# Performance work log

Measured on AMD Instinct MI355X. Metric: run time of the kernel, lower is better.

## Reference

```python
import jax, jax.numpy as jnp
import numpy as np

PI = float(np.pi)


def _lsa_cols(cost):
    """Jonker-Volgenant / Hungarian on a square cost matrix (numpy float64).
    Returns col_ind such that (arange(n), col_ind) is the optimal assignment,
    matching scipy.optimize.linear_sum_assignment for a square matrix."""
    n = cost.shape[0]
    C = np.zeros((n + 1, n + 1), dtype=np.float64)
    C[1:, 1:] = cost
    u = np.zeros(n + 1)
    v = np.zeros(n + 1)
    p = np.zeros(n + 1, dtype=np.int64)  # p[j] = row matched to column j (1-indexed)
    for i in range(1, n + 1):
        p[0] = i
        j0 = 0
        minv = np.full(n + 1, np.inf)
        way = np.zeros(n + 1, dtype=np.int64)
        used = np.zeros(n + 1, dtype=bool)
        while True:
            used[j0] = True
            i0 = p[j0]
            cur = C[i0] - u[i0] - v
            upd = (~used) & (cur < minv)
            minv = np.where(upd, cur, minv)
            way[upd] = j0
            masked = np.where(used, np.inf, minv)
            j1 = int(np.argmin(masked))
            delta = masked[j1]
            u[p[used]] += delta
            v[used] -= delta
            minv[~used] -= delta
            j0 = j1
            if p[j0] == 0:
                break
        while j0:
            j1 = way[j0]
            p[j0] = p[j1]
            j0 = j1
    col_to_row = p[1:] - 1  # row assigned to each column
    col_ind = np.empty(n, dtype=np.int64)
    col_ind[col_to_row] = np.arange(n)
    return col_ind


def _batched_assignment(input, target):
    # cdist p=2 : (B, N, N)
    diff = input[:, :, None, :] - target[:, None, :, :]
    cost = jnp.sqrt(jnp.sum(diff * diff, axis=-1))
    cost_np = np.asarray(cost, dtype=np.float64)
    # serial per-sample Hungarian solve (mirrors the original scipy loop)
    cols = np.stack([_lsa_cols(cost_np[b]) for b in range(cost_np.shape[0])], axis=0)
    return jnp.asarray(cols)  # (B, N)


def setup_inputs() -> dict:
    key = jax.random.key(0)
    k1, k2 = jax.random.split(key)
    B, N, D = 128, 128, 5
    return {
        "input": jax.random.normal(k1, (B, N, D), dtype=jnp.float32),
        "target": jax.random.normal(k2, (B, N, D), dtype=jnp.float32),
    }


def reference(input, target):
    cols = _batched_assignment(input, target)  # (B, N), constant w.r.t. grads
    # row_ind is identity (square matrix), so aligned_pred == input;
    # aligned_true = target gathered by the optimal columns.
    aligned_true = jnp.take_along_axis(target, cols[:, :, None], axis=1)
    d = input - aligned_true
    x_loss = jnp.mean(d[..., 0] ** 2)
    y_loss = jnp.mean(d[..., 1] ** 2)
    E_loss = jnp.mean(d[..., 2] ** 2)
    theta_loss = jnp.mean(d[..., 3] ** 2)
    phi_diff = jnp.remainder(d[..., 4] + PI, 2.0 * PI) - PI  # wrap to (-pi, pi]
    phi_loss = jnp.mean(phi_diff ** 2)
    total_loss = x_loss + y_loss + E_loss + theta_loss + phi_loss
    # [total, x, y, E, theta, phi]
    return jnp.stack([total_loss, x_loss, y_loss, E_loss, theta_loss, phi_loss])
```

## Files before the change

### kernel.cpp

```cpp
#include <hip/hip_runtime.h>

#define NN 128
#define NB 128
#define ND 5
#define INFV 3.4028235e38f

__device__ __forceinline__ float wrap_phi(float x) {
  const float PI_F   = 3.14159265358979323846f;
  const float TWO_PI = 6.28318530717958647692f;
  float t = x + PI_F;
  float w = t - floorf(t * (1.0f / TWO_PI)) * TWO_PI;
  return w - PI_F;
}

#define DPP_SRC_INF(x, ctrl, rmask)                                           \
  __int_as_float(__builtin_amdgcn_update_dpp(                                 \
      0x7f800000, __float_as_int(x), (ctrl), (rmask), 0xF, false))

#define DPP_MIN_STEP(x, ctrl, rmask) x = fminf(x, DPP_SRC_INF(x, ctrl, rmask))

#define DPP_MIN2_STEP(x1, x2, ctrl, rmask)                                    \
  { float _a1 = DPP_SRC_INF(x1, ctrl, rmask);                                 \
    float _a2 = DPP_SRC_INF(x2, ctrl, rmask);                                 \
    float _t  = fmaxf(x1, _a1);                                               \
    x1 = fminf(x1, _a1);                                                      \
    x2 = fminf(fminf(x2, _a2), _t); }

__device__ __forceinline__ int rl_i(int v, int lane) {
  return __builtin_amdgcn_readlane(v, lane);
}
__device__ __forceinline__ float rl_f(float v, int lane) {
  return __int_as_float(__builtin_amdgcn_readlane(__float_as_int(v), lane));
}

__device__ __forceinline__ float wave_min_bcast(float x) {
  DPP_MIN_STEP(x, 0xB1,  0xF);
  DPP_MIN_STEP(x, 0x4E,  0xF);
  DPP_MIN_STEP(x, 0x141, 0xF);
  DPP_MIN_STEP(x, 0x140, 0xF);
  DPP_MIN_STEP(x, 0x142, 0xA);
  DPP_MIN_STEP(x, 0x143, 0xC);
  return rl_f(x, 63);
}

__device__ __forceinline__ void wave_min2_bcast(float &x1, float &x2) {
  DPP_MIN2_STEP(x1, x2, 0xB1,  0xF);
  DPP_MIN2_STEP(x1, x2, 0x4E,  0xF);
  DPP_MIN2_STEP(x1, x2, 0x141, 0xF);
  DPP_MIN2_STEP(x1, x2, 0x140, 0xF);
  DPP_MIN2_STEP(x1, x2, 0x142, 0xA);
  DPP_MIN2_STEP(x1, x2, 0x143, 0xC);
  x1 = rl_f(x1, 63);
  x2 = rl_f(x2, 63);
}

__global__ __launch_bounds__(64) void set2set_hungarian(
    const float* __restrict__ inp, const float* __restrict__ tgt,
    float* __restrict__ sums)
{
  const int b = blockIdx.x;
  const int lane = threadIdx.x;

  __shared__ __align__(16) float Csh[NN * NN];
  __shared__ float inpS[NN * ND];
  __shared__ int   rowOwner[NN + 1];
  __shared__ float uFree[NN + 1];

  const float* inB = inp + (size_t)b * NN * ND;
  const float* tgB = tgt + (size_t)b * NN * ND;

  for (int idx = lane; idx < NN * ND; idx += 64) inpS[idx] = inB[idx];
  for (int idx = lane; idx <= NN; idx += 64) { rowOwner[idx] = 0x7fffffff; uFree[idx] = 0.f; }
  __syncthreads();

  const int jA = 2 * lane;
  const int jB = 2 * lane + 1;
  const int c1A = jA + 1, c1B = jB + 1;

  float tA[ND], tB[ND];
  #pragma unroll
  for (int d = 0; d < ND; ++d) { tA[d] = tgB[jA * ND + d]; tB[d] = tgB[jB * ND + d]; }

  float vA = INFV, vB = INFV;
  int   rmA = 1,  rmB = 1;
  #pragma unroll 4
  for (int i = 0; i < NN; ++i) {
    float sA = 0.f, sB = 0.f;
    #pragma unroll
    for (int d = 0; d < ND; ++d) {
      float x = inpS[i * ND + d];
      float da = x - tA[d]; sA = fmaf(da, da, sA);
      float db = x - tB[d]; sB = fmaf(db, db, sB);
    }
    float cA = sqrtf(sA), cB = sqrtf(sB);
    ((float2*)(Csh + i * NN))[lane] = make_float2(cA, cB);
    if (cA < vA) { vA = cA; rmA = i + 1; }
    if (cB < vB) { vB = cB; rmB = i + 1; }
  }
  __syncthreads();

  atomicMin(&rowOwner[rmA], c1A);
  atomicMin(&rowOwner[rmB], c1B);
  __syncthreads();

  int   pA = (rowOwner[rmA] == c1A) ? rmA : 0;
  int   pB = (rowOwner[rmB] == c1B) ? rmB : 0;
  float uA = 0.f, uB = 0.f;
  int   wayA = 0, wayB = 0;

  {
    const float vOldA = vA, vOldB = vB;
    unsigned long long mtA = __ballot(pA != 0);
    unsigned long long mtB = __ballot(pB != 0);
    while (mtA | mtB) {
      int l1, s1;
      if (mtA) { l1 = __ffsll(mtA) - 1; mtA &= mtA - 1ull; s1 = 0; }
      else     { l1 = __ffsll(mtB) - 1; mtB &= mtB - 1ull; s1 = 1; }
      int i1 = rl_i(s1 ? pB : pA, l1);
      int l2 = -1, s2 = 0, i2 = 0;
      if (mtA)      { l2 = __ffsll(mtA) - 1; mtA &= mtA - 1ull; s2 = 0; }
      else if (mtB) { l2 = __ffsll(mtB) - 1; mtB &= mtB - 1ull; s2 = 1; }
      if (l2 >= 0) i2 = rl_i(s2 ? pB : pA, l2);

      const float2 c1 = ((const float2*)(Csh + (i1 - 1) * NN))[lane];
      float2 c2 = make_float2(0.f, 0.f);
      if (i2) c2 = ((const float2*)(Csh + (i2 - 1) * NN))[lane];

      float r1A = c1.x - vOldA, r1B = c1.y - vOldB;
      if (lane == l1) { if (s1) r1B = INFV; else r1A = INFV; }
      float mu1 = wave_min_bcast(fminf(r1A, r1B));
      bool e1A = (lane == l1) && (s1 == 0);
      bool e1B = (lane == l1) && (s1 == 1);
      vA -= e1A ? mu1 : 0.f;   vB -= e1B ? mu1 : 0.f;
      uA  = e1A ? mu1 : uA;    uB  = e1B ? mu1 : uB;

      if (i2) {
        float r2A = c2.x - vOldA, r2B = c2.y - vOldB;
        if (lane == l2) { if (s2) r2B = INFV; else r2A = INFV; }
        float mu2 = wave_min_bcast(fminf(r2A, r2B));
        bool e2A = (lane == l2) && (s2 == 0);
        bool e2B = (lane == l2) && (s2 == 1);
        vA -= e2A ? mu2 : 0.f;   vB -= e2B ? mu2 : 0.f;
        uA  = e2A ? mu2 : uA;    uB  = e2B ? mu2 : uB;
      }
    }
  }

  unsigned long long remLo = __ballot(rowOwner[1 + lane]  == 0x7fffffff);
  unsigned long long remHi = __ballot(rowOwner[65 + lane] == 0x7fffffff);

  #pragma unroll 1
  for (int pass = 0; pass < 8; ++pass) {
    unsigned long long inLo = remLo, inHi = remHi;
    unsigned long long outLo = 0ull, outHi = 0ull;
    while (inLo | inHi) {
      int i;
      if (inLo) { int t = __ffsll(inLo) - 1; inLo &= inLo - 1ull; i = t + 1; }
      else      { int t = __ffsll(inHi) - 1; inHi &= inHi - 1ull; i = t + 65; }

      const float2 c = ((const float2*)(Csh + (i - 1) * NN))[lane];
      float rcA = c.x - vA, rcB = c.y - vB;
      float m1 = fminf(rcA, rcB), m2 = fmaxf(rcA, rcB);
      float candv = m1;
      bool  aMin  = (rcA <= rcB);
      int   candc = aMin ? c1A : c1B;
      int   candp = aMin ? pA : pB;
      float candu = aMin ? uA : uB;
      wave_min2_bcast(m1, m2);

      unsigned long long msk = __ballot(candv == m1);
      int l = __ffsll(msk) - 1;
      int   j1   = rl_i(candc, l);
      int   i0   = rl_i(candp, l);
      float uOld = rl_f(candu, l);
      int owner = l, slot = (j1 - 1) & 1;

      float dv = m2 - m1;
      bool selA = (lane == owner) && (slot == 0);
      bool selB = (lane == owner) && (slot == 1);
      vA -= selA ? dv : 0.f;   vB -= selB ? dv : 0.f;
      pA  = selA ? i  : pA;    pB  = selB ? i  : pB;
      uA  = selA ? m2 : uA;    uB  = selB ? m2 : uB;

      if (i0 != 0) {
        if (lane == 0) uFree[i0] = uOld;
        if (i0 <= 64) outLo |= 1ull << (i0 - 1);
        else          outHi |= 1ull << (i0 - 65);
      }
    }
    remLo = outLo; remHi = outHi;
  }
  unsigned long long dijLo = remLo, dijHi = remHi;

  while (dijLo | dijHi) {
    int i;
    if (dijLo) { int t = __ffsll(dijLo) - 1; dijLo &= dijLo - 1ull; i = t + 1; }
    else       { int t = __ffsll(dijHi) - 1; dijHi &= dijHi - 1ull; i = t + 65; }
    float uf = uFree[i];

    float dLiveA = INFV, dLiveB = INFV;
    float dFrzA = 0.f, dFrzB = 0.f;
    bool usedA = false, usedB = false;
    int   j0 = 0, i0 = i;
    float minVal = 0.f;
    float tshift = 0.f - uf;
    float tvA = tshift - vA, tvB = tshift - vB;
    int   jfree = 0;

    for (int guard = 0; guard <= NN + 1; ++guard) {
      const float2 c = ((const float2*)(Csh + (i0 - 1) * NN))[lane];
      float curA = c.x + tvA;
      float curB = c.y + tvB;
      float curMA = usedA ? INFV : curA;
      float curMB = usedB ? INFV : curB;
      bool okA = curMA < dLiveA;
      bool okB = curMB < dLiveB;
      wayA = okA ? j0 : wayA;
      wayB = okB ? j0 : wayB;
      dLiveA = fminf(dLiveA, curMA);
      dLiveB = fminf(dLiveB, curMB);

      float candv = fminf(dLiveA, dLiveB);
      bool  aMin  = (dLiveA <= dLiveB);
      int   candc = aMin ? c1A : c1B;
      int   candp = aMin ? pA : pB;
      float candu = aMin ? uA : uB;

      minVal = wave_min_bcast(candv);
      unsigned long long msk = __ballot(candv == minVal);
      int l = __ffsll(msk) - 1;
      int   j1  = rl_i(candc, l);
      int   pj1 = rl_i(candp, l);
      float uj  = rl_f(candu, l);
      if (pj1 == 0) { jfree = j1; break; }

      bool nowA = (j1 == c1A), nowB = (j1 == c1B);
      usedA |= nowA;  usedB |= nowB;
      dFrzA = nowA ? minVal : dFrzA;
      dFrzB = nowB ? minVal : dFrzB;
      dLiveA = nowA ? INFV : dLiveA;
      dLiveB = nowB ? INFV : dLiveB;
      tshift = minVal - uj;
      tvA = tshift - vA;  tvB = tshift - vB;
      j0 = j1; i0 = pj1;
    }

    {
      float adjA = dFrzA - minVal;
      float adjB = dFrzB - minVal;
      vA += usedA ? adjA : 0.f;   uA -= usedA ? adjA : 0.f;
      vB += usedB ? adjB : 0.f;   uB -= usedB ? adjB : 0.f;
    }
    float ucur = uf + minVal;

    int jj = jfree;
    for (int g = 0; g < NN + 1 && jj != 0; ++g) {
      int owner = (jj - 1) >> 1, slot = (jj - 1) & 1;
      int wj = slot ? rl_i(wayB, owner) : rl_i(wayA, owner);
      int pnew; float unew;
      if (wj == 0) { pnew = i; unew = ucur; }
      else {
        int o2 = (wj - 1) >> 1, s2 = (wj - 1) & 1;
        pnew = s2 ? rl_i(pB, o2) : rl_i(pA, o2);
        unew = s2 ? rl_f(uB, o2) : rl_f(uA, o2);
      }
      bool selA = (lane == owner) && (slot == 0);
      bool selB = (lane == owner) && (slot == 1);
      pA = selA ? pnew : pA;  uA = selA ? unew : uA;
      pB = selB ? pnew : pB;  uB = selB ? unew : uB;
      jj = wj;
    }
  }

  int rA = pA - 1;
  int rB = pB - 1;
  float acc[ND];
  #pragma unroll
  for (int d = 0; d < ND; ++d) {
    float dA = inpS[rA * ND + d] - tA[d];
    float dB = inpS[rB * ND + d] - tB[d];
    if (d == 4) { dA = wrap_phi(dA); dB = wrap_phi(dB); }
    acc[d] = dA * dA + dB * dB;
  }
  #pragma unroll
  for (int d = 0; d < ND; ++d) {
    float s = acc[d];
    #pragma unroll
    for (int off = 32; off > 0; off >>= 1) s += __shfl_xor(s, off);
    if (lane == 0) atomicAdd(&sums[d], s);
  }
}

__global__ void set2set_finalize(const float* __restrict__ sums, float* __restrict__ out) {
  const float inv = 1.0f / (128.0f * 128.0f);
  float x  = sums[0] * inv;
  float y  = sums[1] * inv;
  float E  = sums[2] * inv;
  float th = sums[3] * inv;
  float ph = sums[4] * inv;
  out[1] = x; out[2] = y; out[3] = E; out[4] = th; out[5] = ph;
  out[0] = x + y + E + th + ph;
}

extern "C" void kernel_launch(void* const* d_in, const int* in_sizes, int n_in,
                              void* d_out, int out_size, void* d_ws, size_t ws_size,
                              hipStream_t stream) {
  const float* inp = (const float*)d_in[0];
  const float* tgt = (const float*)d_in[1];
  float* out  = (float*)d_out;
  float* sums = (float*)d_ws;

  hipMemsetAsync(sums, 0, ND * sizeof(float), stream);
  set2set_hungarian<<<dim3(NB), dim3(64), 0, stream>>>(inp, tgt, sums);
  set2set_finalize<<<dim3(1), dim3(1), 0, stream>>>(sums, out);
}
```

Baseline: 378.6 us.

## Speculatively prefetch cost row for second-smallest column in Dijkstra loop

Each augmenting-path step now computes a wave-wide top-2 minimum instead of a single minimum. It identifies the runner-up column and preloads that column's owner row from shared memory. If the next step selects that column, the cost row is already in registers and the shared-memory load drops off the critical dependency chain. The price is an extra two-value reduction, extra ballots and readlanes, and a speculative LDS load on every iteration, which may cost more than the latency it hides.

```diff
diff --git a/kernel.cpp b/kernel.cpp
--- a/kernel.cpp
+++ b/kernel.cpp
@@ -206,9 +206,16 @@
     float tshift = 0.f - uf;
     float tvA = tshift - vA, tvB = tshift - vB;
     int   jfree = 0;
+    int   specJ = -1;
+    float2 specRow = make_float2(0.f, 0.f);
 
     for (int guard = 0; guard <= NN + 1; ++guard) {
-      const float2 c = ((const float2*)(Csh + (i0 - 1) * NN))[lane];
+      float2 c;
+      if (j0 == specJ) {
+        c = specRow;
+      } else {
+        c = ((const float2*)(Csh + (i0 - 1) * NN))[lane];
+      }
       float curA = c.x + tvA;
       float curB = c.y + tvB;
       float curMA = usedA ? INFV : curA;
@@ -220,14 +227,18 @@
       dLiveA = fminf(dLiveA, curMA);
       dLiveB = fminf(dLiveB, curMB);
 
-      float candv = fminf(dLiveA, dLiveB);
-      bool  aMin  = (dLiveA <= dLiveB);
-      int   candc = aMin ? c1A : c1B;
-      int   candp = aMin ? pA : pB;
-      float candu = aMin ? uA : uB;
-
-      minVal = wave_min_bcast(candv);
-      unsigned long long msk = __ballot(candv == minVal);
+      float m1l = fminf(dLiveA, dLiveB);
+      float m2l = fmaxf(dLiveA, dLiveB);
+      bool  aMin   = (dLiveA <= dLiveB);
+      int   candc  = aMin ? c1A : c1B;
+      int   candcO = aMin ? c1B : c1A;
+      int   candp  = aMin ? pA : pB;
+      float candu  = aMin ? uA : uB;
+
+      float r1 = m1l, r2 = m2l;
+      wave_min2_bcast(r1, r2);
+      minVal = r1;
+      unsigned long long msk = __ballot(m1l == minVal);
       int l = __ffsll(msk) - 1;
       int   j1  = rl_i(candc, l);
       int   pj1 = rl_i(candp, l);
@@ -243,6 +254,24 @@
       tshift = minVal - uj;
       tvA = tshift - vA;  tvB = tshift - vB;
       j0 = j1; i0 = pj1;
+
+      specJ = -1;
+      if (r2 < INFV) {
+        unsigned long long g1 = __ballot(m1l == r2) & ~(1ull << l);
+        unsigned long long g2 = __ballot(m2l == r2);
+        int jg = 0;
+        if (g1)      { int lg = __ffsll(g1) - 1; jg = rl_i(candc,  lg); }
+        else if (g2) { int lg = __ffsll(g2) - 1; jg = rl_i(candcO, lg); }
+        if (jg == j1) jg = 0;
+        if (jg) {
+          int og = (jg - 1) >> 1, sg = (jg - 1) & 1;
+          int pg = rl_i(sg ? pB : pA, og);
+          if (pg != 0) {
+            specJ = jg;
+            specRow = ((const float2*)(Csh + (pg - 1) * NN))[lane];
+          }
+        }
+      }
     }
 
     {
```

New measurement: 466.3 us. 23.1% more time.
